# Kernel optimization log

Hardware: AMD Instinct MI355X
Metric: run time of the kernel (lower is better)

## Reference

```python
import jax, jax.numpy as jnp
import numpy as np

G1 = 3.0  # cfg.TRAIN.IoU_Gamma1
G2 = 1.0  # cfg.TRAIN.IoU_Gamma2


def setup_inputs() -> dict:
    key = jax.random.key(0)
    ks = jax.random.split(key, 5)
    B, N = 16, 2048
    cls = 0.3 * jax.random.normal(ks[0], (B, N, 2), jnp.float32)
    label_cls = jax.random.randint(ks[1], (B, N), 0, 2).astype(jnp.int32)
    label_loc = jax.random.normal(ks[2], (B, 4, N), jnp.float32)
    pred_bboxes = jax.random.uniform(ks[3], (B, 4, N), jnp.float32)
    label_target = jax.random.uniform(ks[4], (B, 4), jnp.float32)
    dataset_id = jnp.zeros((B,), jnp.int32)
    return dict(cls=cls, label_cls=label_cls, label_loc=label_loc,
                pred_bboxes=pred_bboxes, label_target=label_target,
                dataset_id=dataset_id)


def _iou(boxes, target):
    # boxes [B,4,N] (x1,y1,x2,y2); target [B,4]
    x1, y1, x2, y2 = boxes[:, 0], boxes[:, 1], boxes[:, 2], boxes[:, 3]
    tx1, ty1, tx2, ty2 = (target[:, 0:1], target[:, 1:2],
                          target[:, 2:3], target[:, 3:4])
    ww = jnp.clip(jnp.minimum(tx2, x2) - jnp.maximum(tx1, x1), 0.0)
    hh = jnp.clip(jnp.minimum(ty2, y2) - jnp.maximum(ty1, y1), 0.0)
    area = (x2 - x1) * (y2 - y1)
    ta = (tx2 - tx1) * (ty2 - ty1)
    inter = ww * hh
    return inter / (area + ta - inter)  # [B,N]


def _forward(cls, label_loc, pred_bboxes, label_target, label_cls, dataset_id):
    prob = jnp.exp(cls[..., 1])                      # [B,N]
    pos = label_cls > 0                              # [B,N]
    iou = _iou(pred_bboxes, label_target)            # [B,N]
    # centerness distance to target center
    cx = label_loc[:, 0] + label_target[:, 0:1]      # [B,N]
    cy = label_loc[:, 1] + label_target[:, 1:2]
    tcx = (label_target[:, 0] + label_target[:, 2]) * 0.5
    tcy = (label_target[:, 1] + label_target[:, 3]) * 0.5
    d = jnp.sqrt((cx - tcx[:, None]) ** 2 + (cy - tcy[:, None]) ** 2)  # [B,N]
    # pair (p,q): both positive, d[q]-d[p] >= 1.0 (== nested sorted-loop selection)
    pair = (pos[:, :, None] & pos[:, None, :]
            & ((d[:, None, :] - d[:, :, None]) >= 1.0))               # [B,N,N]
    m = pair.astype(prob.dtype)
    cnt = m.sum((1, 2))                                               # [B]
    # guard exponent with the mask to avoid inf*0 on dead pairs
    e1 = jnp.where(pair, -G1 * (prob[:, :, None] - prob[:, None, :]), 0.0)
    iou_sg = jax.lax.stop_gradient(iou)
    e2 = jnp.where(pair, -G2 * (iou[:, :, None] - iou_sg[:, None, :]), 0.0)
    denom = jnp.maximum(cnt, 1.0)
    l1 = (jnp.exp(e1) * m).sum((1, 2)) / denom                        # [B]
    l2 = (jnp.exp(e2) * m).sum((1, 2)) / denom
    valid = ((dataset_id != 1) & (cnt > 0)).astype(prob.dtype)        # [B]
    nv = valid.sum()
    safe_nv = jnp.maximum(nv, 1.0)
    f1 = jnp.where(nv > 0, (l1 * valid).sum() / safe_nv, 0.0)
    f2 = jnp.where(nv > 0, (l2 * valid).sum() / safe_nv, 0.0)
    return (f1, f2)


def reference(cls, label_cls, label_loc, pred_bboxes, label_target, dataset_id):
    return _forward(cls, label_loc, pred_bboxes, label_target, label_cls, dataset_id)
```

## Files before the change

### kernel.cpp

```cpp
#include <hip/hip_runtime.h>


#define G1 3.0f
#define G2 1.0f

constexpr int B    = 16;
constexpr int N    = 2048;
constexpr int TJ   = 64;
constexpr int IPT  = 4;
constexpr int TI   = 1024;
constexpr int ICH  = N / TI;
constexpr int JCH  = N / TJ;
constexpr int PB   = ICH * JCH;
constexpr int NBLK = B * PB;

__global__ void __launch_bounds__(256)
pair_kernel(const float* __restrict__ cls, const int* __restrict__ label_cls,
            const float* __restrict__ label_loc, const float* __restrict__ pred,
            const float* __restrict__ tgt, double* __restrict__ part) {
  __shared__ uint4  stile[TJ];
  __shared__ float  ssd[TJ];
  __shared__ float  suf1[TJ + 1], suf2[TJ + 1];
  __shared__ double red[3][4];

  const int bid = blockIdx.x;
  const int b   = bid >> 6;
  const int r   = bid & 63;
  const int ic  = r >> 5;
  const int jc  = r & 31;
  const int t   = threadIdx.x;
  const int base = b * N;

  const float tx1 = tgt[b * 4 + 0], ty1 = tgt[b * 4 + 1];
  const float tx2 = tgt[b * 4 + 2], ty2 = tgt[b * 4 + 3];
  const float ta  = (tx2 - tx1) * (ty2 - ty1);
  const float tcx = (tx1 + tx2) * 0.5f, tcy = (ty1 + ty2) * 0.5f;

  const float* __restrict__ pb = pred      + (size_t)b * 4 * N;
  const float* __restrict__ lb = label_loc + (size_t)b * 4 * N;

  auto elem = [&](int n, float& d, float& prob, float& iou, bool& pos) {
    float x1 = pb[n], y1 = pb[N + n], x2 = pb[2 * N + n], y2 = pb[3 * N + n];
    float ww = fmaxf(fminf(tx2, x2) - fmaxf(tx1, x1), 0.f);
    float hh = fmaxf(fminf(ty2, y2) - fmaxf(ty1, y1), 0.f);
    float inter = ww * hh;
    iou  = inter / ((x2 - x1) * (y2 - y1) + ta - inter);
    prob = __expf(cls[((size_t)(base + n)) * 2 + 1]);
    pos  = label_cls[base + n] > 0;
    float cx = lb[n] + tx1, cy = lb[N + n] + ty1;
    float dx = cx - tcx, dy = cy - tcy;
    d = sqrtf(dx * dx + dy * dy);
  };

  float dm_j = 0.f; unsigned uj = 0u;
  if (t < TJ) {
    float d, prob, iou; bool pos;
    elem(jc * TJ + t, d, prob, iou, pos);
    dm_j = pos ? d : -1e30f;
    uj = __float_as_uint(dm_j);
    uj ^= (uj & 0x80000000u) ? 0xFFFFFFFFu : 0x80000000u;
    stile[t] = make_uint4(uj, (unsigned)t,
                          __float_as_uint(__expf(G1 * prob)),
                          __float_as_uint(__expf(G2 * iou)));
  }
  if (t == TJ) { suf1[TJ] = 0.f; suf2[TJ] = 0.f; }

  float di[IPT], v1i[IPT], v2i[IPT];
#pragma unroll
  for (int k = 0; k < IPT; ++k) {
    float d, prob, iou; bool pos;
    elem(ic * TI + k * 256 + t, d, prob, iou, pos);
    di[k]  = d;
    v1i[k] = pos ? __expf(-G1 * prob) : 0.f;
    v2i[k] = pos ? __expf(-G2 * iou)  : 0.f;
  }
  __syncthreads();

  if (t < TJ) {
    const unsigned long long mykey = ((unsigned long long)uj << 32) | (unsigned)t;
    int rank = 0; float s1 = 0.f, s2 = 0.f;
#pragma unroll 8
    for (int q = 0; q < TJ; ++q) {
      uint4 v = stile[q];
      unsigned long long kq = ((unsigned long long)v.x << 32) | v.y;
      bool lt = kq < mykey;
      rank += lt ? 1 : 0;
      s1 += lt ? 0.f : __uint_as_float(v.z);
      s2 += lt ? 0.f : __uint_as_float(v.w);
    }
    ssd[rank] = dm_j; suf1[rank] = s1; suf2[rank] = s2;
  }
  __syncthreads();

  double p1 = 0.0, p2 = 0.0; int cnt = 0;
#pragma unroll
  for (int k = 0; k < IPT; ++k) {
    const float d = di[k];
    int kk = 0;
#pragma unroll
    for (int w = TJ >> 1; w > 0; w >>= 1)
      kk += (ssd[kk + w - 1] - d >= 1.0f) ? 0 : w;
    kk += (ssd[kk] - d >= 1.0f) ? 0 : 1;
    p1 += (double)v1i[k] * (double)suf1[kk];
    p2 += (double)v2i[k] * (double)suf2[kk];
    cnt += (v1i[k] > 0.f) ? (TJ - kk) : 0;
  }
  double pc = (double)cnt;

  for (int off = 32; off; off >>= 1) {
    p1 += __shfl_down(p1, off);
    p2 += __shfl_down(p2, off);
    pc += __shfl_down(pc, off);
  }
  const int wv = t >> 6, lane = t & 63;
  if (lane == 0) { red[0][wv] = p1; red[1][wv] = p2; red[2][wv] = pc; }
  __syncthreads();
  if (t == 0) {
    part[(size_t)bid * 3 + 0] = red[0][0] + red[0][1] + red[0][2] + red[0][3];
    part[(size_t)bid * 3 + 1] = red[1][0] + red[1][1] + red[1][2] + red[1][3];
    part[(size_t)bid * 3 + 2] = red[2][0] + red[2][1] + red[2][2] + red[2][3];
  }
}

__global__ void finalize_kernel(const double* __restrict__ part,
                                const int* __restrict__ dataset_id,
                                float* __restrict__ out) {
  __shared__ double sl1[B], sl2[B], sv[B];
  int t = threadIdx.x;
  int b = t >> 4, k = t & 15;

  double s1 = 0, s2 = 0, sc = 0;
#pragma unroll
  for (int q = 0; q < PB; q += 16) {
    size_t idx = (size_t)(b * PB + k + q) * 3;
    s1 += part[idx]; s2 += part[idx + 1]; sc += part[idx + 2];
  }
  for (int off = 8; off; off >>= 1) {
    s1 += __shfl_down(s1, off, 16);
    s2 += __shfl_down(s2, off, 16);
    sc += __shfl_down(sc, off, 16);
  }
  if (k == 0) {
    double denom = fmax(sc, 1.0);
    bool valid = (dataset_id[b] != 1) && (sc > 0.0);
    sl1[b] = valid ? s1 / denom : 0.0;
    sl2[b] = valid ? s2 / denom : 0.0;
    sv[b]  = valid ? 1.0 : 0.0;
  }
  __syncthreads();
  if (t == 0) {
    double nv = 0, f1 = 0, f2 = 0;
    for (int bb = 0; bb < B; ++bb) { nv += sv[bb]; f1 += sl1[bb]; f2 += sl2[bb]; }
    out[0] = (float)((nv > 0) ? f1 / nv : 0.0);
    out[1] = (float)((nv > 0) ? f2 / nv : 0.0);
  }
}

extern "C" void kernel_launch(void* const* d_in, const int* in_sizes, int n_in,
                              void* d_out, int out_size, void* d_ws, size_t ws_size,
                              hipStream_t stream) {
  const float* cls       = (const float*)d_in[0];
  const int*   label_cls = (const int*)d_in[1];
  const float* label_loc = (const float*)d_in[2];
  const float* pred      = (const float*)d_in[3];
  const float* tgt       = (const float*)d_in[4];
  const int*   dset      = (const int*)d_in[5];

  double* part = (double*)d_ws;

  pair_kernel<<<NBLK, 256, 0, stream>>>(cls, label_cls, label_loc, pred, tgt, part);
  finalize_kernel<<<1, 256, 0, stream>>>(part, dset, (float*)d_out);
}
```

Baseline: 16.64 us.

## Cover full i-range per block and vectorize per-element loads with float4

Each block now handles all 2048 i-elements of its batch (8 per thread) against one 64-wide j tile, which halves the block count and the redundant j-tile setup and sort. The per-element input loads are changed to float4/int4 vector loads, so each thread processes 4 contiguous elements per load group. The trade-off is fewer blocks (512) with more work per thread and higher register use, which may reduce latency hiding.

```diff
diff --git a/kernel.cpp b/kernel.cpp
--- a/kernel.cpp
+++ b/kernel.cpp
@@ -7,12 +7,9 @@
 constexpr int B    = 16;
 constexpr int N    = 2048;
 constexpr int TJ   = 64;
-constexpr int IPT  = 4;
-constexpr int TI   = 1024;
-constexpr int ICH  = N / TI;
+constexpr int IPT  = 8;
 constexpr int JCH  = N / TJ;
-constexpr int PB   = ICH * JCH;
-constexpr int NBLK = B * PB;
+constexpr int NBLK = B * JCH;
 
 __global__ void __launch_bounds__(256)
 pair_kernel(const float* __restrict__ cls, const int* __restrict__ label_cls,
@@ -23,12 +20,10 @@
   __shared__ float  suf1[TJ + 1], suf2[TJ + 1];
   __shared__ double red[3][4];
 
-  const int bid = blockIdx.x;
-  const int b   = bid >> 6;
-  const int r   = bid & 63;
-  const int ic  = r >> 5;
-  const int jc  = r & 31;
-  const int t   = threadIdx.x;
+  const int bid  = blockIdx.x;
+  const int b    = bid >> 5;
+  const int jc   = bid & 31;
+  const int t    = threadIdx.x;
   const int base = b * N;
 
   const float tx1 = tgt[b * 4 + 0], ty1 = tgt[b * 4 + 1];
@@ -39,23 +34,19 @@
   const float* __restrict__ pb = pred      + (size_t)b * 4 * N;
   const float* __restrict__ lb = label_loc + (size_t)b * 4 * N;
 
-  auto elem = [&](int n, float& d, float& prob, float& iou, bool& pos) {
+  float dm_j = 0.f; unsigned uj = 0u;
+  if (t < TJ) {
+    const int n = jc * TJ + t;
     float x1 = pb[n], y1 = pb[N + n], x2 = pb[2 * N + n], y2 = pb[3 * N + n];
     float ww = fmaxf(fminf(tx2, x2) - fmaxf(tx1, x1), 0.f);
     float hh = fmaxf(fminf(ty2, y2) - fmaxf(ty1, y1), 0.f);
     float inter = ww * hh;
-    iou  = inter / ((x2 - x1) * (y2 - y1) + ta - inter);
-    prob = __expf(cls[((size_t)(base + n)) * 2 + 1]);
-    pos  = label_cls[base + n] > 0;
+    float iou  = inter / ((x2 - x1) * (y2 - y1) + ta - inter);
+    float prob = __expf(cls[((size_t)(base + n)) * 2 + 1]);
+    bool  pos  = label_cls[base + n] > 0;
     float cx = lb[n] + tx1, cy = lb[N + n] + ty1;
     float dx = cx - tcx, dy = cy - tcy;
-    d = sqrtf(dx * dx + dy * dy);
-  };
-
-  float dm_j = 0.f; unsigned uj = 0u;
-  if (t < TJ) {
-    float d, prob, iou; bool pos;
-    elem(jc * TJ + t, d, prob, iou, pos);
+    float d  = sqrtf(dx * dx + dy * dy);
     dm_j = pos ? d : -1e30f;
     uj = __float_as_uint(dm_j);
     uj ^= (uj & 0x80000000u) ? 0xFFFFFFFFu : 0x80000000u;
@@ -65,14 +56,48 @@
   }
   if (t == TJ) { suf1[TJ] = 0.f; suf2[TJ] = 0.f; }
 
+  const float4* __restrict__ pb4 = (const float4*)pb;
+  const float4* __restrict__ lb4 = (const float4*)lb;
+  const float4* __restrict__ cl4 = (const float4*)(cls + (size_t)base * 2);
+  const int4*   __restrict__ lc4 = (const int4*)(label_cls + base);
+
   float di[IPT], v1i[IPT], v2i[IPT];
 #pragma unroll
-  for (int k = 0; k < IPT; ++k) {
-    float d, prob, iou; bool pos;
-    elem(ic * TI + k * 256 + t, d, prob, iou, pos);
-    di[k]  = d;
-    v1i[k] = pos ? __expf(-G1 * prob) : 0.f;
-    v2i[k] = pos ? __expf(-G2 * iou)  : 0.f;
+  for (int h = 0; h < 2; ++h) {
+    const int w = h * 256 + t;
+    const float4 X1 = pb4[0 * (N / 4) + w];
+    const float4 Y1 = pb4[1 * (N / 4) + w];
+    const float4 X2 = pb4[2 * (N / 4) + w];
+    const float4 Y2 = pb4[3 * (N / 4) + w];
+    const float4 CX = lb4[0 * (N / 4) + w];
+    const float4 CY = lb4[1 * (N / 4) + w];
+    const float4 C0 = cl4[2 * w + 0];
+    const float4 C1 = cl4[2 * w + 1];
+    const int4   LC = lc4[w];
+    const float x1v[4] = {X1.x, X1.y, X1.z, X1.w};
+    const float y1v[4] = {Y1.x, Y1.y, Y1.z, Y1.w};
+    const float x2v[4] = {X2.x, X2.y, X2.z, X2.w};
+    const float y2v[4] = {Y2.x, Y2.y, Y2.z, Y2.w};
+    const float cxv[4] = {CX.x, CX.y, CX.z, CX.w};
+    const float cyv[4] = {CY.x, CY.y, CY.z, CY.w};
+    const float clv[4] = {C0.y, C0.w, C1.y, C1.w};
+    const int   lcv[4] = {LC.x, LC.y, LC.z, LC.w};
+#pragma unroll
+    for (int c = 0; c < 4; ++c) {
+      const int k = h * 4 + c;
+      float x1 = x1v[c], y1 = y1v[c], x2 = x2v[c], y2 = y2v[c];
+      float ww = fmaxf(fminf(tx2, x2) - fmaxf(tx1, x1), 0.f);
+      float hh = fmaxf(fminf(ty2, y2) - fmaxf(ty1, y1), 0.f);
+      float inter = ww * hh;
+      float iou  = inter / ((x2 - x1) * (y2 - y1) + ta - inter);
+      float prob = __expf(clv[c]);
+      bool  pos  = lcv[c] > 0;
+      float cx = cxv[c] + tx1, cy = cyv[c] + ty1;
+      float dx = cx - tcx, dy = cy - tcy;
+      di[k]  = sqrtf(dx * dx + dy * dy);
+      v1i[k] = pos ? __expf(-G1 * prob) : 0.f;
+      v2i[k] = pos ? __expf(-G2 * iou)  : 0.f;
+    }
   }
   __syncthreads();
 
@@ -131,8 +156,8 @@
 
   double s1 = 0, s2 = 0, sc = 0;
 #pragma unroll
-  for (int q = 0; q < PB; q += 16) {
-    size_t idx = (size_t)(b * PB + k + q) * 3;
+  for (int q = 0; q < JCH; q += 16) {
+    size_t idx = (size_t)(b * JCH + k + q) * 3;
     s1 += part[idx]; s2 += part[idx + 1]; sc += part[idx + 2];
   }
   for (int off = 8; off; off >>= 1) {
```

New measurement: 18.97 us. +14.0%, slower.
